# Kernel optimization log

Hardware: AMD Instinct MI355X
Metric: run time of the kernel (lower is better)

Reference implementation:

```python
import jax, jax.numpy as jnp
import numpy as np
from jax import lax

WH, WW = 8, 8            # window_size
NUM_HEADS = 6
DIM = 192

def _rel_index(wh, ww):
    # static relative-position index table, [N, N] with N = wh*ww
    ch = np.arange(wh); cw = np.arange(ww)
    coords = np.stack(np.meshgrid(ch, cw, indexing='ij')).reshape(2, -1)  # [2, N]
    rel = (coords[:, :, None] - coords[:, None, :]).transpose(1, 2, 0).astype(np.int64)  # [N,N,2]
    rel[:, :, 0] += wh - 1
    rel[:, :, 1] += ww - 1
    rel[:, :, 0] *= 2 * ww - 1
    return jnp.asarray(rel.sum(-1))

REL_IDX = _rel_index(WH, WW)  # [64, 64] int

def _conv(x, w, b, groups=1):
    # NCHW conv, SAME padding, stride 1
    y = lax.conv_general_dilated(x, w, (1, 1), 'SAME',
                                 dimension_numbers=('NCHW', 'OIHW', 'NCHW'),
                                 feature_group_count=groups)
    return y + b[None, :, None, None]

def setup_inputs() -> dict:
    key = jax.random.key(0)
    ks = jax.random.split(key, 8)
    b, nW = 2048, 512
    x = jax.random.normal(ks[0], (b, WH, WW, DIM), jnp.float32)
    mask = jax.random.normal(ks[1], (nW, WH * WW, WH * WW), jnp.float32)
    qkv_w = jax.random.normal(ks[2], (3 * DIM, DIM, 1, 1), jnp.float32) * 0.02
    qkv_b = jnp.zeros((3 * DIM,), jnp.float32)
    dw_w = jax.random.normal(ks[3], (3 * DIM, 1, 3, 3), jnp.float32) * 0.02  # depthwise, groups = 3*dim
    dw_b = jnp.zeros((3 * DIM,), jnp.float32)
    proj_w = jax.random.normal(ks[4], (DIM, DIM, 1, 1), jnp.float32) * 0.02
    proj_b = jnp.zeros((DIM,), jnp.float32)
    temperature = jnp.ones((NUM_HEADS, 1, 1), jnp.float32)
    rel_bias_table = jax.random.normal(ks[5], ((2 * WH - 1) * (2 * WW - 1), NUM_HEADS), jnp.float32) * 0.02
    return {"x": x, "mask": mask, "qkv_w": qkv_w, "qkv_b": qkv_b, "dw_w": dw_w,
            "dw_b": dw_b, "proj_w": proj_w, "proj_b": proj_b,
            "temperature": temperature, "rel_bias_table": rel_bias_table}

def reference(x, mask, qkv_w, qkv_b, dw_w, dw_b, proj_w, proj_b, temperature, rel_bias_table):
    b, h, w, c = x.shape
    n = h * w
    ch = c // NUM_HEADS
    xc = jnp.transpose(x, (0, 3, 1, 2))                      # [b, c, h, w]
    qkv = _conv(_conv(xc, qkv_w, qkv_b), dw_w, dw_b, groups=3 * c)
    q, k, v = jnp.split(qkv, 3, axis=1)

    def to_heads(t):  # [b, c, h, w] -> [b, head, n, c_head]
        return t.reshape(b, NUM_HEADS, ch, n).transpose(0, 1, 3, 2)

    q, k, v = to_heads(q), to_heads(k), to_heads(v)
    q = q / jnp.maximum(jnp.linalg.norm(q, axis=-1, keepdims=True), 1e-12)
    k = k / jnp.maximum(jnp.linalg.norm(k, axis=-1, keepdims=True), 1e-12)

    attn = jnp.einsum('bhnc,bhmc->bhnm', q, k) * temperature[None]   # cosine sim * learned temp
    bias = rel_bias_table[REL_IDX]                                   # [n, n, head]
    attn = attn + jnp.transpose(bias, (2, 0, 1))[None]

    nW = mask.shape[0]
    attn = attn.reshape(b // nW, nW, NUM_HEADS, n, n) + mask[None, :, None]
    attn = jax.nn.softmax(attn.reshape(b, NUM_HEADS, n, n), axis=-1)

    out = jnp.einsum('bhnm,bhmc->bhnc', attn, v)
    out = out.transpose(0, 1, 3, 2).reshape(b, c, h, w)              # b (head c) h w
    return _conv(out, proj_w, proj_b)                                # [b, c, h, w]
```

## Files before the change

kernel.cpp:

```cpp
#include <hip/hip_runtime.h>

typedef unsigned short u16;
typedef unsigned int   u32;
typedef __attribute__((ext_vector_type(8))) short bf16x8;
typedef __attribute__((ext_vector_type(4))) float f32x4;

#define STR_XS 200
#define STR_LB 68
#define STR_Q  72

__device__ u16   g_wq[576 * 192];
__device__ u16   g_wp[192 * 192];
__device__ float g_bh[6 * 64 * 64];
__device__ float g_dwt[10 * 576];

__device__ __forceinline__ u32 pkbf(float lo, float hi) {
    return __builtin_amdgcn_perm(__float_as_uint(hi) + 0x8000u,
                                 __float_as_uint(lo) + 0x8000u, 0x07060302u);
}
__device__ __forceinline__ u16 sbf(float f) {
    return (u16)((__float_as_uint(f) + 0x8000u) >> 16);
}

__global__ __launch_bounds__(256) void prep(
    const float* __restrict__ qkv_w, const float* __restrict__ proj_w,
    const float* __restrict__ btab, const float* __restrict__ dw_w,
    const float* __restrict__ dw_b)
{
    int i = blockIdx.x * 256 + threadIdx.x;
    if (i < 110592) { g_wq[i] = sbf(qkv_w[i]); return; }
    i -= 110592;
    if (i < 36864) { g_wp[i] = sbf(proj_w[i]); return; }
    i -= 36864;
    if (i < 24576) {
        int h = i >> 12, m = (i >> 6) & 63, n = i & 63;
        int ry = (m >> 3) - (n >> 3) + 7, rx = (m & 7) - (n & 7) + 7;
        g_bh[i] = btab[(ry * 15 + rx) * 6 + h];
        return;
    }
    i -= 24576;
    if (i < 5760) {
        int tap = i / 576, o = i - tap * 576;
        g_dwt[i] = (tap < 9) ? dw_w[o * 9 + tap] : dw_b[o];
    }
}

__global__ __launch_bounds__(256, 2) void wattn(
    const float* __restrict__ x, const float* __restrict__ mask,
    const float* __restrict__ qkv_b, const float* __restrict__ temp,
    const float* __restrict__ proj_b, float* __restrict__ out, int nW)
{
    const int b    = blockIdx.x;
    const int tid  = threadIdx.x;
    const int lane = tid & 63;
    const int wid  = __builtin_amdgcn_readfirstlane(tid >> 6);
    const int quad = lane >> 4, l15 = lane & 15;

    __shared__ u16   xs[64 * STR_XS];
    __shared__ float arena[64 * STR_LB];
    __shared__ u16   qh[64 * STR_Q];
    __shared__ u16   kh[64 * STR_Q];
    __shared__ u16   vh[64 * STR_Q];
    __shared__ u16   oh[64 * STR_Q];

    {
        const float* xb = x + (size_t)b * 12288;
        #pragma unroll
        for (int r = 0; r < 12; ++r) {
            int i4 = tid + r * 256;
            int pp = i4 / 48, c0 = (i4 % 48) * 4;
            float4 v = *(const float4*)(xb + pp * 192 + c0);
            u32* d = (u32*)&xs[pp * STR_XS + c0];
            d[0] = pkbf(v.x, v.y);
            d[1] = pkbf(v.z, v.w);
        }
    }

    const float* gmask = mask + (size_t)(b % nW) * 4096;
    const int p  = wid * 16 + l15;
    const int py = p >> 3, px = p & 7;

    f32x4 accP[12];
    #pragma unroll
    for (int i = 0; i < 12; ++i) accP[i] = f32x4{0.f, 0.f, 0.f, 0.f};

    for (int it = 0; it < 3; ++it) {
        for (int g = 0; g < 3; ++g) {
            const int obase = g * 192 + it * 64;
            __syncthreads();
            {
                f32x4 C[4];
                #pragma unroll
                for (int mt = 0; mt < 4; ++mt) C[mt] = f32x4{0.f, 0.f, 0.f, 0.f};
                const u16* wb = g_wq + (size_t)(obase + wid * 16 + l15) * 192;
                #pragma unroll
                for (int kf = 0; kf < 6; ++kf) {
                    bf16x8 bw = *(const bf16x8*)(wb + kf * 32 + quad * 8);
                    #pragma unroll
                    for (int mt = 0; mt < 4; ++mt) {
                        bf16x8 a = *(const bf16x8*)&xs[(mt * 16 + l15) * STR_XS + kf * 32 + quad * 8];
                        C[mt] = __builtin_amdgcn_mfma_f32_16x16x32_bf16(a, bw, C[mt], 0, 0, 0);
                    }
                }
                float qb = qkv_b[obase + wid * 16 + l15];
                #pragma unroll
                for (int mt = 0; mt < 4; ++mt)
                    #pragma unroll
                    for (int r = 0; r < 4; ++r)
                        arena[(mt * 16 + quad * 4 + r) * STR_LB + wid * 16 + l15] = C[mt][r] + qb;
            }
            __syncthreads();
            const int c0 = quad * 16;
            const float* dwt = g_dwt + obase + c0;
            float dwv[16];
            {
                const float* bs = dwt + 9 * 576;
                *(f32x4*)&dwv[0]  = *(const f32x4*)(bs);
                *(f32x4*)&dwv[4]  = *(const f32x4*)(bs + 4);
                *(f32x4*)&dwv[8]  = *(const f32x4*)(bs + 8);
                *(f32x4*)&dwv[12] = *(const f32x4*)(bs + 12);
            }
            #pragma unroll
            for (int dy = -1; dy <= 1; ++dy) {
                int yy = py + dy;
                if ((unsigned)yy < 8u) {
                    #pragma unroll
                    for (int dx = -1; dx <= 1; ++dx) {
                        int xx = px + dx;
                        if ((unsigned)xx < 8u) {
                            const float* src = &arena[(yy * 8 + xx) * STR_LB + c0];
                            const float* wt  = dwt + ((dy + 1) * 3 + dx + 1) * 576;
                            float nb[16], wv[16];
                            *(f32x4*)&nb[0]  = *(const f32x4*)(src);
                            *(f32x4*)&nb[4]  = *(const f32x4*)(src + 4);
                            *(f32x4*)&nb[8]  = *(const f32x4*)(src + 8);
                            *(f32x4*)&nb[12] = *(const f32x4*)(src + 12);
                            *(f32x4*)&wv[0]  = *(const f32x4*)(wt);
                            *(f32x4*)&wv[4]  = *(const f32x4*)(wt + 4);
                            *(f32x4*)&wv[8]  = *(const f32x4*)(wt + 8);
                            *(f32x4*)&wv[12] = *(const f32x4*)(wt + 12);
                            #pragma unroll
                            for (int j = 0; j < 16; ++j)
                                dwv[j] = fmaf(nb[j], wv[j], dwv[j]);
                        }
                    }
                }
            }
            if (g < 2) {
                float ss = 0.f;
                #pragma unroll
                for (int j = 0; j < 16; ++j) ss = fmaf(dwv[j], dwv[j], ss);
                ss += __shfl_xor(ss, 16, 64);
                float tf = (g == 0) ? temp[it * 2 + (quad >> 1)] : 1.f;
                float s = tf / fmaxf(sqrtf(ss), 1e-12f);
                u16* dst = (g == 0) ? qh : kh;
                u32* d = (u32*)&dst[p * STR_Q + c0];
                #pragma unroll
                for (int j = 0; j < 8; ++j)
                    d[j] = pkbf(dwv[2 * j] * s, dwv[2 * j + 1] * s);
            } else {
                #pragma unroll
                for (int j = 0; j < 16; ++j)
                    vh[(c0 + j) * STR_Q + p] = sbf(dwv[j]);
            }
        }
        __syncthreads();

        u16* Pw = ((u16*)arena) + wid * (16 * STR_Q);
        for (int h2 = 0; h2 < 2; ++h2) {
            const int h = it * 2 + h2, ch0 = h2 * 32;
            f32x4 S[4];
            #pragma unroll
            for (int nt = 0; nt < 4; ++nt) S[nt] = f32x4{0.f, 0.f, 0.f, 0.f};
            bf16x8 aq = *(const bf16x8*)&qh[(wid * 16 + l15) * STR_Q + ch0 + quad * 8];
            #pragma unroll
            for (int nt = 0; nt < 4; ++nt) {
                bf16x8 bk = *(const bf16x8*)&kh[(nt * 16 + l15) * STR_Q + ch0 + quad * 8];
                S[nt] = __builtin_amdgcn_mfma_f32_16x16x32_bf16(aq, bk, S[nt], 0, 0, 0);
            }
            const float* bh = g_bh + h * 4096 + (wid * 16 + quad * 4) * 64 + l15;
            const float* gm = gmask + (wid * 16 + quad * 4) * 64 + l15;
            #pragma unroll
            for (int nt = 0; nt < 4; ++nt)
                #pragma unroll
                for (int r = 0; r < 4; ++r)
                    S[nt][r] += bh[r * 64 + nt * 16] + gm[r * 64 + nt * 16];
            #pragma unroll
            for (int r = 0; r < 4; ++r) {
                float mx = fmaxf(fmaxf(S[0][r], S[1][r]), fmaxf(S[2][r], S[3][r]));
                mx = fmaxf(mx, __shfl_xor(mx, 1, 64));
                mx = fmaxf(mx, __shfl_xor(mx, 2, 64));
                mx = fmaxf(mx, __shfl_xor(mx, 4, 64));
                mx = fmaxf(mx, __shfl_xor(mx, 8, 64));
                float e0 = __expf(S[0][r] - mx), e1 = __expf(S[1][r] - mx);
                float e2 = __expf(S[2][r] - mx), e3 = __expf(S[3][r] - mx);
                float sm = (e0 + e1) + (e2 + e3);
                sm += __shfl_xor(sm, 1, 64);
                sm += __shfl_xor(sm, 2, 64);
                sm += __shfl_xor(sm, 4, 64);
                sm += __shfl_xor(sm, 8, 64);
                float iv = 1.f / sm;
                u16* pr = Pw + (quad * 4 + r) * STR_Q + l15;
                pr[0]  = sbf(e0 * iv);
                pr[16] = sbf(e1 * iv);
                pr[32] = sbf(e2 * iv);
                pr[48] = sbf(e3 * iv);
            }
            f32x4 O[2];
            O[0] = f32x4{0.f, 0.f, 0.f, 0.f};
            O[1] = f32x4{0.f, 0.f, 0.f, 0.f};
            #pragma unroll
            for (int kf = 0; kf < 2; ++kf) {
                bf16x8 ap = *(const bf16x8*)(Pw + l15 * STR_Q + kf * 32 + quad * 8);
                #pragma unroll
                for (int nt = 0; nt < 2; ++nt) {
                    bf16x8 bv = *(const bf16x8*)&vh[(ch0 + nt * 16 + l15) * STR_Q + kf * 32 + quad * 8];
                    O[nt] = __builtin_amdgcn_mfma_f32_16x16x32_bf16(ap, bv, O[nt], 0, 0, 0);
                }
            }
            #pragma unroll
            for (int nt = 0; nt < 2; ++nt)
                #pragma unroll
                for (int r = 0; r < 4; ++r)
                    oh[(wid * 16 + quad * 4 + r) * STR_Q + ch0 + nt * 16 + l15] = sbf(O[nt][r]);
        }
        __syncthreads();

        #pragma unroll
        for (int kf = 0; kf < 2; ++kf) {
            bf16x8 A4[4];
            #pragma unroll
            for (int mt = 0; mt < 4; ++mt)
                A4[mt] = *(const bf16x8*)&oh[(mt * 16 + l15) * STR_Q + kf * 32 + quad * 8];
            #pragma unroll
            for (int nt = 0; nt < 3; ++nt) {
                bf16x8 bw = *(const bf16x8*)(g_wp + (size_t)(wid * 48 + nt * 16 + l15) * 192 + it * 64 + kf * 32 + quad * 8);
                #pragma unroll
                for (int mt = 0; mt < 4; ++mt)
                    accP[nt * 4 + mt] = __builtin_amdgcn_mfma_f32_16x16x32_bf16(A4[mt], bw, accP[nt * 4 + mt], 0, 0, 0);
            }
        }
    }

    __syncthreads();
    {
        float* ob = out + (size_t)b * 12288;
        for (int rr = 0; rr < 3; ++rr) {
            float pb = proj_b[wid * 48 + rr * 16 + l15];
            #pragma unroll
            for (int mt = 0; mt < 4; ++mt)
                #pragma unroll
                for (int r = 0; r < 4; ++r)
                    arena[(wid * 16 + l15) * STR_LB + mt * 16 + quad * 4 + r] = accP[rr * 4 + mt][r] + pb;
            __syncthreads();
            {
                int ol = tid >> 2, sub = tid & 3;
                int ocg = (ol >> 4) * 48 + rr * 16 + (ol & 15);
                const float4* srp = (const float4*)&arena[ol * STR_LB + sub * 16];
                float4* dst = (float4*)(ob + (size_t)ocg * 64 + sub * 16);
                dst[0] = srp[0]; dst[1] = srp[1]; dst[2] = srp[2]; dst[3] = srp[3];
            }
            __syncthreads();
        }
    }
}

extern "C" void kernel_launch(void* const* d_in, const int* in_sizes, int n_in,
                              void* d_out, int out_size, void* d_ws, size_t ws_size,
                              hipStream_t stream)
{
    const float* x      = (const float*)d_in[0];
    const float* mask   = (const float*)d_in[1];
    const float* qkv_w  = (const float*)d_in[2];
    const float* qkv_b  = (const float*)d_in[3];
    const float* dw_w   = (const float*)d_in[4];
    const float* dw_b   = (const float*)d_in[5];
    const float* proj_w = (const float*)d_in[6];
    const float* proj_b = (const float*)d_in[7];
    const float* temp   = (const float*)d_in[8];
    const float* btab   = (const float*)d_in[9];
    float* out = (float*)d_out;

    const int b  = in_sizes[0] / 12288;
    const int nW = in_sizes[1] / 4096;

    prep<<<dim3(695), dim3(256), 0, stream>>>(qkv_w, proj_w, btab, dw_w, dw_b);
    wattn<<<dim3(b), dim3(256), 0, stream>>>(x, mask, qkv_b, temp, proj_b, out, nW);
}
```

Before: 419.3 us.

## Restructure QKV GEMM operand roles and register-block depthwise conv over pixels

The QKV pointwise GEMM now takes the weights as the A operand, prefetched from global memory into 24 registers before the barrier, and reads x from LDS as the B operand. The output goes to the arena as vectorized float4 stores in pixel-major layout instead of scalar transposed stores. The depthwise 3x3 conv is reorganised so each lane handles 4 channels over 4 adjacent pixels in a row. This lets neighbouring pixels share loaded neighbour vectors, with tap weights held in registers. The channel norm now uses a 3-step shuffle reduction and V is written with packed stores. The aim is fewer LDS and global loads and less per-pixel redundancy, at the cost of higher register pressure from the Aw and wt arrays.

```diff
diff --git a/kernel.cpp b/kernel.cpp
--- a/kernel.cpp
+++ b/kernel.cpp
@@ -77,8 +77,11 @@
     }
 
     const float* gmask = mask + (size_t)(b % nW) * 4096;
-    const int p  = wid * 16 + l15;
-    const int py = p >> 3, px = p & 7;
+    const int pyd = wid * 2 + (lane >> 5);
+    const int td  = (lane >> 4) & 1;
+    const int cg  = lane & 15;
+    const int c0d = cg * 4;
+    const int px0 = td * 4;
 
     f32x4 accP[12];
     #pragma unroll
@@ -87,81 +90,97 @@
     for (int it = 0; it < 3; ++it) {
         for (int g = 0; g < 3; ++g) {
             const int obase = g * 192 + it * 64;
+            bf16x8 Aw[24];
+            {
+                const u16* wb = g_wq + (size_t)obase * 192 + (size_t)l15 * 192 + quad * 8;
+                #pragma unroll
+                for (int mt = 0; mt < 4; ++mt)
+                    #pragma unroll
+                    for (int kf = 0; kf < 6; ++kf)
+                        Aw[mt * 6 + kf] = *(const bf16x8*)(wb + mt * 3072 + kf * 32);
+            }
             __syncthreads();
             {
                 f32x4 C[4];
                 #pragma unroll
                 for (int mt = 0; mt < 4; ++mt) C[mt] = f32x4{0.f, 0.f, 0.f, 0.f};
-                const u16* wb = g_wq + (size_t)(obase + wid * 16 + l15) * 192;
                 #pragma unroll
                 for (int kf = 0; kf < 6; ++kf) {
-                    bf16x8 bw = *(const bf16x8*)(wb + kf * 32 + quad * 8);
+                    bf16x8 bx = *(const bf16x8*)&xs[(wid * 16 + l15) * STR_XS + kf * 32 + quad * 8];
                     #pragma unroll
-                    for (int mt = 0; mt < 4; ++mt) {
-                        bf16x8 a = *(const bf16x8*)&xs[(mt * 16 + l15) * STR_XS + kf * 32 + quad * 8];
-                        C[mt] = __builtin_amdgcn_mfma_f32_16x16x32_bf16(a, bw, C[mt], 0, 0, 0);
+                    for (int mt = 0; mt < 4; ++mt)
+                        C[mt] = __builtin_amdgcn_mfma_f32_16x16x32_bf16(Aw[mt * 6 + kf], bx, C[mt], 0, 0, 0);
+                }
+                #pragma unroll
+                for (int mt = 0; mt < 4; ++mt) {
+                    f32x4 qb = *(const f32x4*)(qkv_b + obase + mt * 16 + quad * 4);
+                    f32x4 o;
+                    o.x = C[mt].x + qb.x; o.y = C[mt].y + qb.y;
+                    o.z = C[mt].z + qb.z; o.w = C[mt].w + qb.w;
+                    *(f32x4*)&arena[(wid * 16 + l15) * STR_LB + mt * 16 + quad * 4] = o;
+                }
+            }
+            __syncthreads();
+            f32x4 wt[9];
+            #pragma unroll
+            for (int tap = 0; tap < 9; ++tap)
+                wt[tap] = *(const f32x4*)(g_dwt + tap * 576 + obase + c0d);
+            f32x4 dacc[4];
+            {
+                f32x4 bsv = *(const f32x4*)(g_dwt + 9 * 576 + obase + c0d);
+                #pragma unroll
+                for (int i = 0; i < 4; ++i) dacc[i] = bsv;
+            }
+            #pragma unroll
+            for (int dy = -1; dy <= 1; ++dy) {
+                int yy = pyd + dy;
+                if ((unsigned)yy < 8u) {
+                    f32x4 nb[6];
+                    #pragma unroll
+                    for (int j = 0; j < 6; ++j) {
+                        int xx = px0 - 1 + j;
+                        if ((unsigned)xx < 8u)
+                            nb[j] = *(const f32x4*)&arena[(yy * 8 + xx) * STR_LB + c0d];
+                        else
+                            nb[j] = f32x4{0.f, 0.f, 0.f, 0.f};
                     }
-                }
-                float qb = qkv_b[obase + wid * 16 + l15];
-                #pragma unroll
-                for (int mt = 0; mt < 4; ++mt)
                     #pragma unroll
-                    for (int r = 0; r < 4; ++r)
-                        arena[(mt * 16 + quad * 4 + r) * STR_LB + wid * 16 + l15] = C[mt][r] + qb;
-            }
-            __syncthreads();
-            const int c0 = quad * 16;
-            const float* dwt = g_dwt + obase + c0;
-            float dwv[16];
-            {
-                const float* bs = dwt + 9 * 576;
-                *(f32x4*)&dwv[0]  = *(const f32x4*)(bs);
-                *(f32x4*)&dwv[4]  = *(const f32x4*)(bs + 4);
-                *(f32x4*)&dwv[8]  = *(const f32x4*)(bs + 8);
-                *(f32x4*)&dwv[12] = *(const f32x4*)(bs + 12);
-            }
-            #pragma unroll
-            for (int dy = -1; dy <= 1; ++dy) {
-                int yy = py + dy;
-                if ((unsigned)yy < 8u) {
-                    #pragma unroll
-                    for (int dx = -1; dx <= 1; ++dx) {
-                        int xx = px + dx;
-                        if ((unsigned)xx < 8u) {
-                            const float* src = &arena[(yy * 8 + xx) * STR_LB + c0];
-                            const float* wt  = dwt + ((dy + 1) * 3 + dx + 1) * 576;
-                            float nb[16], wv[16];
-                            *(f32x4*)&nb[0]  = *(const f32x4*)(src);
-                            *(f32x4*)&nb[4]  = *(const f32x4*)(src + 4);
-                            *(f32x4*)&nb[8]  = *(const f32x4*)(src + 8);
-                            *(f32x4*)&nb[12] = *(const f32x4*)(src + 12);
-                            *(f32x4*)&wv[0]  = *(const f32x4*)(wt);
-                            *(f32x4*)&wv[4]  = *(const f32x4*)(wt + 4);
-                            *(f32x4*)&wv[8]  = *(const f32x4*)(wt + 8);
-                            *(f32x4*)&wv[12] = *(const f32x4*)(wt + 12);
-                            #pragma unroll
-                            for (int j = 0; j < 16; ++j)
-                                dwv[j] = fmaf(nb[j], wv[j], dwv[j]);
+                    for (int i = 0; i < 4; ++i)
+                        #pragma unroll
+                        for (int dxp = 0; dxp < 3; ++dxp) {
+                            f32x4 w = wt[(dy + 1) * 3 + dxp];
+                            f32x4 nv = nb[i + dxp];
+                            dacc[i].x = fmaf(nv.x, w.x, dacc[i].x);
+                            dacc[i].y = fmaf(nv.y, w.y, dacc[i].y);
+                            dacc[i].z = fmaf(nv.z, w.z, dacc[i].z);
+                            dacc[i].w = fmaf(nv.w, w.w, dacc[i].w);
                         }
-                    }
                 }
             }
             if (g < 2) {
-                float ss = 0.f;
-                #pragma unroll
-                for (int j = 0; j < 16; ++j) ss = fmaf(dwv[j], dwv[j], ss);
-                ss += __shfl_xor(ss, 16, 64);
-                float tf = (g == 0) ? temp[it * 2 + (quad >> 1)] : 1.f;
-                float s = tf / fmaxf(sqrtf(ss), 1e-12f);
+                float tf = (g == 0) ? temp[it * 2 + (cg >> 3)] : 1.f;
                 u16* dst = (g == 0) ? qh : kh;
-                u32* d = (u32*)&dst[p * STR_Q + c0];
-                #pragma unroll
-                for (int j = 0; j < 8; ++j)
-                    d[j] = pkbf(dwv[2 * j] * s, dwv[2 * j + 1] * s);
+                #pragma unroll
+                for (int i = 0; i < 4; ++i) {
+                    float s = dacc[i].x * dacc[i].x;
+                    s = fmaf(dacc[i].y, dacc[i].y, s);
+                    s = fmaf(dacc[i].z, dacc[i].z, s);
+                    s = fmaf(dacc[i].w, dacc[i].w, s);
+                    s += __shfl_xor(s, 1, 64);
+                    s += __shfl_xor(s, 2, 64);
+                    s += __shfl_xor(s, 4, 64);
+                    float sc = tf / fmaxf(sqrtf(s), 1e-12f);
+                    u32* d = (u32*)&dst[(pyd * 8 + px0 + i) * STR_Q + c0d];
+                    d[0] = pkbf(dacc[i].x * sc, dacc[i].y * sc);
+                    d[1] = pkbf(dacc[i].z * sc, dacc[i].w * sc);
+                }
             } else {
                 #pragma unroll
-                for (int j = 0; j < 16; ++j)
-                    vh[(c0 + j) * STR_Q + p] = sbf(dwv[j]);
+                for (int j = 0; j < 4; ++j) {
+                    u32* d = (u32*)&vh[(c0d + j) * STR_Q + pyd * 8 + px0];
+                    d[0] = pkbf(dacc[0][j], dacc[1][j]);
+                    d[1] = pkbf(dacc[2][j], dacc[3][j]);
+                }
             }
         }
         __syncthreads();
```

Result: slower. 486.7 us (+16.1%).
